# Performance work log

Measured on AMD Instinct MI355X. Metric: run time of the kernel, lower is better.

## Reference

```python
import jax, jax.numpy as jnp
import numpy as np
import math

B, T, D = 2, 2048, 2048
N_HEADS, N_KV, HEAD_DIM = 16, 4, 128
INTER = 8192
MAX_POS = 4096
ROPE_BASE = 10000.0
EPS = 1e-6


def _rope_tables():
    inv_freq = 1.0 / (ROPE_BASE ** (jnp.arange(0, HEAD_DIM, 2, dtype=jnp.float32) / HEAD_DIM))
    t = jnp.arange(MAX_POS, dtype=jnp.float32)
    freqs = jnp.einsum('i,j->ij', t, inv_freq)          # [MAX_POS, HEAD_DIM//2]
    emb = jnp.concatenate([freqs, freqs], axis=-1)      # [MAX_POS, HEAD_DIM]
    return jnp.cos(emb), jnp.sin(emb)


def _apply_rope(x, cos, sin):
    # x: [B,H,T,Dh]; cos/sin: [B,T,Dh] (gathered by position_ids)
    c = cos[:, None, :, :]
    s = sin[:, None, :, :]
    x1 = x[..., ::2]
    x2 = x[..., 1::2]
    x_rot = jnp.stack([-x2, x1], axis=-1).reshape(x.shape)  # interleave(-x2, x1)
    return x * c + x_rot * s


def _rms_norm(x, w):
    var = jnp.mean(x * x, axis=-1, keepdims=True)
    return w * (x * jax.lax.rsqrt(var + EPS))


def setup_inputs() -> dict:
    key = jax.random.key(0)
    ks = jax.random.split(key, 10)
    s = 0.02
    hidden_states = jax.random.normal(ks[0], (B, T, D), dtype=jnp.float32)
    # additive causal mask
    causal = jnp.tril(jnp.ones((T, T), dtype=bool))
    attention_mask = jnp.where(causal, 0.0, -1e9).astype(jnp.float32)[None, None]
    position_ids = jnp.arange(B * T).reshape(B, T)  # values < MAX_POS
    return {
        'hidden_states': hidden_states,
        'attention_mask': attention_mask,
        'position_ids': position_ids,
        'attn_norm_w': jnp.ones((D,), jnp.float32),
        'mlp_norm_w': jnp.ones((D,), jnp.float32),
        'wq': jax.random.normal(ks[1], (D, N_HEADS * HEAD_DIM), jnp.float32) * s,
        'wk': jax.random.normal(ks[2], (D, N_KV * HEAD_DIM), jnp.float32) * s,
        'wv': jax.random.normal(ks[3], (D, N_KV * HEAD_DIM), jnp.float32) * s,
        'wo': jax.random.normal(ks[4], (N_HEADS * HEAD_DIM, D), jnp.float32) * s,
        'gate_w': jax.random.normal(ks[5], (D, D), jnp.float32) * s,
        'gate_b': jnp.zeros((D,), jnp.float32),
        'fc1_w': jax.random.normal(ks[6], (D, INTER), jnp.float32) * s,
        'fc2_w': jax.random.normal(ks[7], (INTER, D), jnp.float32) * s,
    }


def reference(hidden_states, attention_mask, position_ids, attn_norm_w, mlp_norm_w,
              wq, wk, wv, wo, gate_w, gate_b, fc1_w, fc2_w):
    b, t, _ = hidden_states.shape
    residual = hidden_states
    h = _rms_norm(hidden_states, attn_norm_w)

    # elementwise sigmoid output gate: [B,T,D] -> [B,H,T,Dh]
    gate = jax.nn.sigmoid(h @ gate_w + gate_b)
    gate = gate.reshape(b, t, N_HEADS, HEAD_DIM).transpose(0, 2, 1, 3)

    q = (h @ wq).reshape(b, t, N_HEADS, HEAD_DIM).transpose(0, 2, 1, 3)
    k = (h @ wk).reshape(b, t, N_KV, HEAD_DIM).transpose(0, 2, 1, 3)
    v = (h @ wv).reshape(b, t, N_KV, HEAD_DIM).transpose(0, 2, 1, 3)

    cos_t, sin_t = _rope_tables()
    cos = cos_t[position_ids]  # [B,T,Dh]
    sin = sin_t[position_ids]
    q = _apply_rope(q, cos, sin)
    k = _apply_rope(k, cos, sin)

    n_rep = N_HEADS // N_KV
    k = jnp.repeat(k, n_rep, axis=1)  # GQA expand to [B,H,T,Dh]
    v = jnp.repeat(v, n_rep, axis=1)

    scores = jnp.einsum('bhqd,bhkd->bhqk', q, k) / math.sqrt(HEAD_DIM)
    scores = scores + attention_mask
    attn = jax.nn.softmax(scores, axis=-1)
    out = jnp.einsum('bhqk,bhkd->bhqd', attn, v) * gate
    out = out.transpose(0, 2, 1, 3).reshape(b, t, N_HEADS * HEAD_DIM) @ wo

    h = residual + out
    residual = h
    h2 = _rms_norm(h, mlp_norm_w)
    mlp_out = jax.nn.silu(h2 @ fc1_w) @ fc2_w
    return residual + mlp_out
```

## Files before the change

### kernel.cpp

```cpp
#include <hip/hip_runtime.h>
#include <hip/hip_bf16.h>
#include <cstdint>
#include <cstddef>

#define BB 2
#define TT 2048
#define DD 2048
#define NH 16
#define NKV 4
#define HD 128
#define NI 8192
#define MM (BB*TT)

typedef __bf16 bf16x8 __attribute__((ext_vector_type(8)));
typedef float  f32x4  __attribute__((ext_vector_type(4)));

__device__ __forceinline__ void gload_lds16(const void* g, void* l) {
  __builtin_amdgcn_global_load_lds((__attribute__((address_space(1))) void*)g,
                                   (__attribute__((address_space(3))) void*)l,
                                   16, 0, 0);
}

__device__ __forceinline__ int xcd_swizzle(int wg, int nwg) {
  int xcd = wg & 7;
  int l = wg >> 3;
  int q = nwg >> 3, r = nwg & 7;
  return (xcd < r ? xcd * (q + 1) : r * (q + 1) + (xcd - r) * q) + l;
}

__global__ __launch_bounds__(128) void rope_tables_k(float* __restrict__ cosT,
                                                     float* __restrict__ sinT) {
  int pos = blockIdx.x;
  int d = threadIdx.x;
  int f = d & 63;
  float inv = powf(10000.0f, -((float)(2 * f)) / 128.0f);
  float ang = inv * (float)pos;
  cosT[pos * 128 + d] = cosf(ang);
  sinT[pos * 128 + d] = sinf(ang);
}

template <typename TIN>
__global__ __launch_bounds__(256) void transpose_to_bf16_k(const TIN* __restrict__ in,
                                                           __bf16* __restrict__ out,
                                                           int R, int C) {
  __shared__ float t[32][33];
  int c0 = blockIdx.x * 32, r0 = blockIdx.y * 32;
  int tx = threadIdx.x & 31;
  int ty = threadIdx.x >> 5;
#pragma unroll
  for (int i = 0; i < 4; i++) {
    int r = ty + i * 8;
    t[r][tx] = (float)in[(size_t)(r0 + r) * C + c0 + tx];
  }
  __syncthreads();
#pragma unroll
  for (int i = 0; i < 4; i++) {
    int r = ty + i * 8;
    out[(size_t)(c0 + r) * R + r0 + tx] = (__bf16)t[tx][r];
  }
}

__global__ __launch_bounds__(256) void rmsnorm_k(const float* __restrict__ x,
                                                 const float* __restrict__ w,
                                                 __bf16* __restrict__ out) {
  int row = blockIdx.x;
  const float* xr = x + (size_t)row * DD;
  int t = threadIdx.x;
  float4 a = ((const float4*)xr)[2 * t];
  float4 b = ((const float4*)xr)[2 * t + 1];
  float ss = a.x * a.x + a.y * a.y + a.z * a.z + a.w * a.w +
             b.x * b.x + b.y * b.y + b.z * b.z + b.w * b.w;
#pragma unroll
  for (int off = 32; off; off >>= 1) ss += __shfl_xor(ss, off, 64);
  __shared__ float red[4];
  if ((t & 63) == 0) red[t >> 6] = ss;
  __syncthreads();
  float tot = red[0] + red[1] + red[2] + red[3];
  float rs = rsqrtf(tot * (1.0f / DD) + 1e-6f);
  const float4 w1 = ((const float4*)w)[2 * t];
  const float4 w2 = ((const float4*)w)[2 * t + 1];
  bf16x8 ov;
  ov[0] = (__bf16)(a.x * rs * w1.x);
  ov[1] = (__bf16)(a.y * rs * w1.y);
  ov[2] = (__bf16)(a.z * rs * w1.z);
  ov[3] = (__bf16)(a.w * rs * w1.w);
  ov[4] = (__bf16)(b.x * rs * w2.x);
  ov[5] = (__bf16)(b.y * rs * w2.y);
  ov[6] = (__bf16)(b.z * rs * w2.z);
  ov[7] = (__bf16)(b.w * rs * w2.w);
  *(bf16x8*)(out + (size_t)row * DD + t * 8) = ov;
}

enum { G_QG = 0, G_RES = 1, G_SILU = 2, G_PART = 3 };

template <int EPI>
__global__ __launch_bounds__(512) void gemm256_k(
    const __bf16* __restrict__ A, const __bf16* __restrict__ Bt,
    __bf16* __restrict__ outB, float* __restrict__ outF,
    __bf16* __restrict__ outQ, __bf16* __restrict__ outG,
    const float* __restrict__ bias, const float* __restrict__ residual,
    const float* __restrict__ cosT, const float* __restrict__ sinT,
    const int* __restrict__ posids, int N, int K, int ldk, float oscale) {
  __shared__ __align__(16) __bf16 Ab[3][256 * 32];
  __shared__ __align__(16) __bf16 Bb[3][256 * 32];
  const int tid = threadIdx.x;
  const int lane = tid & 63;
  const int wid = tid >> 6;
  const int wr = wid >> 2;
  const int wc = wid & 3;
  const int fr = lane & 15;
  const int fg = lane >> 4;

  const int nwg = gridDim.x * gridDim.y;
  int wg = xcd_swizzle(blockIdx.y * gridDim.x + blockIdx.x, nwg);
  const int bx = wg % gridDim.x, by = wg / gridDim.x;
  const int m0 = by * 256;
  const int n0 = bx * 256;
  const int kz = blockIdx.z;
  const int kBase = kz * K;

  const int srow0 = wid * 32 + (lane >> 2);
  const int scol = (((lane & 3) ^ ((lane >> 3) & 3)) << 3);
  const __bf16* aS0 = A + (size_t)(m0 + srow0) * ldk + kBase + scol;
  const __bf16* aS1 = aS0 + (size_t)16 * ldk;
  const __bf16* bS0 = Bt + (size_t)(n0 + srow0) * ldk + kBase + scol;
  const __bf16* bS1 = bS0 + (size_t)16 * ldk;
  const int e0 = (wid * 2) * 512;
  const int e1 = (wid * 2 + 1) * 512;

  const int nt = K / 32;

#define STAGE_A(kt, s)                          \
  {                                             \
    const int k0_ = (kt) * 32;                  \
    gload_lds16(aS0 + k0_, &Ab[(s)][e0]);       \
    gload_lds16(aS1 + k0_, &Ab[(s)][e1]);       \
  }
#define STAGE_B(kt, s)                          \
  {                                             \
    const int k0_ = (kt) * 32;                  \
    gload_lds16(bS0 + k0_, &Bb[(s)][e0]);       \
    gload_lds16(bS1 + k0_, &Bb[(s)][e1]);       \
  }

  STAGE_A(0, 0);
  STAGE_B(0, 0);
  STAGE_A(1, 1);
  STAGE_B(1, 1);
  asm volatile("s_waitcnt vmcnt(4)" ::: "memory");
  __builtin_amdgcn_s_barrier();

  f32x4 acc[8][4];
#pragma unroll
  for (int i = 0; i < 8; i++)
#pragma unroll
    for (int j = 0; j < 4; j++) acc[i][j] = (f32x4){0.f, 0.f, 0.f, 0.f};

  const int asl = (fg ^ ((fr >> 1) & 3)) * 8;

  for (int t = 0; t < nt; ++t) {
    const int s = t % 3;
    const int sn = (t + 2) % 3;
    bf16x8 af[4], bfr[4];
#pragma unroll
    for (int mi = 0; mi < 4; mi++)
      af[mi] = *(const bf16x8*)&Ab[s][(wr * 128 + mi * 16 + fr) * 32 + asl];
#pragma unroll
    for (int ni = 0; ni < 4; ni++)
      bfr[ni] = *(const bf16x8*)&Bb[s][(wc * 64 + ni * 16 + fr) * 32 + asl];
    if (t + 2 < nt) STAGE_A(t + 2, sn);
    __builtin_amdgcn_s_barrier();
    asm volatile("s_waitcnt lgkmcnt(0)" ::: "memory");
    __builtin_amdgcn_sched_barrier(0);
    __builtin_amdgcn_s_setprio(1);
#pragma unroll
    for (int mi = 0; mi < 4; mi++)
#pragma unroll
      for (int ni = 0; ni < 4; ni++)
        acc[mi][ni] =
            __builtin_amdgcn_mfma_f32_16x16x32_bf16(af[mi], bfr[ni], acc[mi][ni], 0, 0, 0);
    __builtin_amdgcn_s_setprio(0);
    __builtin_amdgcn_s_barrier();
    bf16x8 af2[4];
#pragma unroll
    for (int mi = 0; mi < 4; mi++)
      af2[mi] = *(const bf16x8*)&Ab[s][(wr * 128 + (mi + 4) * 16 + fr) * 32 + asl];
    if (t + 2 < nt) {
      STAGE_B(t + 2, sn);
      asm volatile("s_waitcnt vmcnt(4)" ::: "memory");
    } else {
      asm volatile("s_waitcnt vmcnt(0)" ::: "memory");
    }
    __builtin_amdgcn_s_barrier();
    asm volatile("s_waitcnt lgkmcnt(0)" ::: "memory");
    __builtin_amdgcn_sched_barrier(0);
    __builtin_amdgcn_s_setprio(1);
#pragma unroll
    for (int mi = 0; mi < 4; mi++)
#pragma unroll
      for (int ni = 0; ni < 4; ni++)
        acc[mi + 4][ni] =
            __builtin_amdgcn_mfma_f32_16x16x32_bf16(af2[mi], bfr[ni], acc[mi + 4][ni], 0, 0, 0);
    __builtin_amdgcn_s_setprio(0);
    __builtin_amdgcn_s_barrier();
  }
#undef STAGE_A
#undef STAGE_B

#pragma unroll
  for (int mi = 0; mi < 8; mi++) {
    const int row = m0 + wr * 128 + mi * 16 + fg * 4;
#pragma unroll
    for (int ni = 0; ni < 4; ni++) {
      const int col = n0 + wc * 64 + ni * 16 + fr;
#pragma unroll
      for (int j = 0; j < 4; j++) {
        float v = acc[mi][ni][j];
        const int r = row + j;
        if constexpr (EPI == G_QG) {
          float vp = __shfl_xor(v, 1, 64);
          if (n0 < 2048) {
            int pos = posids[r];
            int d = col & 127;
            float c = cosT[pos * 128 + d], sn2 = sinT[pos * 128 + d];
            float o = (col & 1) ? (v * c + vp * sn2) : (v * c - vp * sn2);
            outQ[(size_t)r * 2048 + col] = (__bf16)(o * oscale);
          } else {
            float xx = v + bias[col - 2048];
            outG[(size_t)r * 2048 + (col - 2048)] = (__bf16)(1.0f / (1.0f + expf(-xx)));
          }
        } else if constexpr (EPI == G_RES) {
          outF[(size_t)r * N + col] = v + residual[(size_t)r * N + col];
        } else if constexpr (EPI == G_SILU) {
          outB[(size_t)r * N + col] = (__bf16)(v / (1.0f + expf(-v)));
        } else {
          outB[(size_t)(kz * MM + r) * N + col] = (__bf16)v;
        }
      }
    }
  }
}

__global__ __launch_bounds__(256) void combine_k(const __bf16* __restrict__ parts,
                                                 const float* __restrict__ res,
                                                 float* __restrict__ out) {
  size_t i = ((size_t)blockIdx.x * 256 + threadIdx.x) * 8;
  bf16x8 p0 = *(const bf16x8*)&parts[i];
  bf16x8 p1 = *(const bf16x8*)&parts[(size_t)MM * 2048 + i];
  float4 a = *(const float4*)&res[i];
  float4 b = *(const float4*)&res[i + 4];
  float4 o0, o1;
  o0.x = (float)p0[0] + (float)p1[0] + a.x;
  o0.y = (float)p0[1] + (float)p1[1] + a.y;
  o0.z = (float)p0[2] + (float)p1[2] + a.z;
  o0.w = (float)p0[3] + (float)p1[3] + a.w;
  o1.x = (float)p0[4] + (float)p1[4] + b.x;
  o1.y = (float)p0[5] + (float)p1[5] + b.y;
  o1.z = (float)p0[6] + (float)p1[6] + b.z;
  o1.w = (float)p0[7] + (float)p1[7] + b.w;
  *(float4*)&out[i] = o0;
  *(float4*)&out[i + 4] = o1;
}

__global__ __launch_bounds__(256) void gemm_kv_k(
    const __bf16* __restrict__ A, const __bf16* __restrict__ Bt,
    __bf16* __restrict__ kOut, __bf16* __restrict__ vOut,
    const float* __restrict__ cosT, const float* __restrict__ sinT,
    const int* __restrict__ posids, int K) {
  __shared__ __align__(16) __bf16 As[128 * 32];
  __shared__ __align__(16) __bf16 Bs[128 * 32];
  const int tid = threadIdx.x;
  const int lane = tid & 63;
  const int w = tid >> 6;
  const int wm = w >> 1, wn = w & 1;

  const int nwg = gridDim.x * gridDim.y;
  int wg = xcd_swizzle(blockIdx.y * gridDim.x + blockIdx.x, nwg);
  const int bx = wg % gridDim.x, by = wg / gridDim.x;
  const int m0 = by * 128;
  const int n0 = bx * 128;

  const int lr = lane >> 2;
  const int lc = (lane & 3) * 8;
  const __bf16* aSrc = A + (size_t)(m0 + 32 * w + lr) * K + lc;
  const __bf16* bSrc = Bt + (size_t)(n0 + 32 * w + lr) * K + lc;
  __bf16* aDst = &As[w * 1024];
  __bf16* bDst = &Bs[w * 1024];

  f32x4 acc[4][4];
#pragma unroll
  for (int i = 0; i < 4; i++)
#pragma unroll
    for (int j = 0; j < 4; j++) acc[i][j] = (f32x4){0.f, 0.f, 0.f, 0.f};

  const int fr = lane & 15;
  const int fc = (lane >> 4) * 8;

  for (int k0 = 0; k0 < K; k0 += 32) {
    __syncthreads();
    gload_lds16(aSrc + k0, aDst);
    gload_lds16(aSrc + k0 + (size_t)16 * K, aDst + 512);
    gload_lds16(bSrc + k0, bDst);
    gload_lds16(bSrc + k0 + (size_t)16 * K, bDst + 512);
    asm volatile("s_waitcnt vmcnt(0)" ::: "memory");
    __syncthreads();

    bf16x8 af[4], bfg[4];
#pragma unroll
    for (int i = 0; i < 4; i++)
      af[i] = *(const bf16x8*)&As[(wm * 64 + i * 16 + fr) * 32 + fc];
#pragma unroll
    for (int i = 0; i < 4; i++)
      bfg[i] = *(const bf16x8*)&Bs[(wn * 64 + i * 16 + fr) * 32 + fc];
#pragma unroll
    for (int mi = 0; mi < 4; mi++)
#pragma unroll
      for (int ni = 0; ni < 4; ni++)
        acc[mi][ni] =
            __builtin_amdgcn_mfma_f32_16x16x32_bf16(af[mi], bfg[ni], acc[mi][ni], 0, 0, 0);
  }

  const int fg = lane >> 4;
#pragma unroll
  for (int mi = 0; mi < 4; mi++) {
#pragma unroll
    for (int ni = 0; ni < 4; ni++) {
#pragma unroll
      for (int j = 0; j < 4; j++) {
        int row = m0 + wm * 64 + mi * 16 + fg * 4 + j;
        int col = n0 + wn * 64 + ni * 16 + fr;
        float v = acc[mi][ni][j];
        float vp = __shfl_xor(v, 1, 64);
        if (col < 512) {
          int pos = posids[row];
          int d = col & 127;
          float c = cosT[pos * 128 + d];
          float s = sinT[pos * 128 + d];
          float o = (col & 1) ? (v * c + vp * s) : (v * c - vp * s);
          kOut[(size_t)row * 512 + col] = (__bf16)o;
        } else {
          vOut[(size_t)row * 512 + (col - 512)] = (__bf16)v;
        }
      }
    }
  }
}

__global__ __launch_bounds__(256) void attn_k(const __bf16* __restrict__ Q,
                                              const __bf16* __restrict__ Kb,
                                              const __bf16* __restrict__ Vt,
                                              const __bf16* __restrict__ Gate,
                                              __bf16* __restrict__ Out) {
  __shared__ __align__(16) __bf16 Ks[2][64 * 128];
  __shared__ __align__(16) __bf16 Vs[2][128 * 64];
  __shared__ __align__(16) __bf16 Ps[4][16 * 64];
  const int tid = threadIdx.x;
  const int lane = tid & 63;
  const int w = tid >> 6;
  const int fr = lane & 15;
  const int fg = lane >> 4;

  const int nwg = gridDim.x * gridDim.y;
  int wg = xcd_swizzle(blockIdx.y * gridDim.x + blockIdx.x, nwg);
  const int qb = wg % gridDim.x;
  const int bh = wg / gridDim.x;
  const int q0 = qb * 64;
  const int b = bh >> 4, h = bh & 15;
  const int g = h >> 2;

  const size_t qrow = (size_t)(b * TT + q0 + w * 16 + fr);
  bf16x8 qf[4];
#pragma unroll
  for (int kt = 0; kt < 4; kt++)
    qf[kt] = *(const bf16x8*)&Q[qrow * 2048 + h * 128 + kt * 32 + fg * 8];

  const __bf16* kPtr[4];
  const __bf16* vPtr[4];
#pragma unroll
  for (int i = 0; i < 4; i++) {
    int krow = w * 16 + i * 4 + (lane >> 4);
    int kcol8 = (lane & 15) ^ (krow & 15);
    kPtr[i] = Kb + (size_t)(b * TT + krow) * 512 + g * 128 + kcol8 * 8;
    int dloc = w * 32 + i * 8 + (lane >> 3);
    int kv8 = (lane & 7) ^ (dloc & 7);
    vPtr[i] = Vt + (size_t)(g * 128 + dloc) * (size_t)MM + b * TT + kv8 * 8;
  }

  f32x4 o[8];
#pragma unroll
  for (int i = 0; i < 8; i++) o[i] = (f32x4){0.f, 0.f, 0.f, 0.f};
  float mrow[4] = {-3e38f, -3e38f, -3e38f, -3e38f};
  float lrow[4] = {0.f, 0.f, 0.f, 0.f};

  const int nsteps = qb + 1;

#pragma unroll
  for (int i = 0; i < 4; i++) {
    gload_lds16(kPtr[i], &Ks[0][w * 2048 + i * 512]);
    gload_lds16(vPtr[i], &Vs[0][w * 2048 + i * 512]);
  }
  __syncthreads();

  for (int t = 0; t < nsteps; t++) {
    const int cur = t & 1;
    const int kb = t * 64;
    if (t + 1 < nsteps) {
      const int nb = kb + 64;
#pragma unroll
      for (int i = 0; i < 4; i++) {
        gload_lds16(kPtr[i] + (size_t)nb * 512, &Ks[cur ^ 1][w * 2048 + i * 512]);
        gload_lds16(vPtr[i] + nb, &Vs[cur ^ 1][w * 2048 + i * 512]);
      }
    }

    f32x4 s[4];
#pragma unroll
    for (int nc = 0; nc < 4; nc++) s[nc] = (f32x4){0.f, 0.f, 0.f, 0.f};
#pragma unroll
    for (int nc = 0; nc < 4; nc++)
#pragma unroll
      for (int kt = 0; kt < 4; kt++) {
        bf16x8 kf = *(const bf16x8*)&Ks[cur][(nc * 16 + fr) * 128 + (((kt * 4 + fg) ^ fr) << 3)];
        s[nc] = __builtin_amdgcn_mfma_f32_16x16x32_bf16(qf[kt], kf, s[nc], 0, 0, 0);
      }

    float alpha[4];
#pragma unroll
    for (int j = 0; j < 4; j++) {
      const int qr = q0 + w * 16 + fg * 4 + j;
      float pv[4];
#pragma unroll
      for (int nc = 0; nc < 4; nc++) {
        int kc = kb + nc * 16 + fr;
        float val = s[nc][j];
        if (kc > qr) val = -1e9f;
        pv[nc] = val;
      }
      float tmx = fmaxf(fmaxf(pv[0], pv[1]), fmaxf(pv[2], pv[3]));
      tmx = fmaxf(tmx, __shfl_xor(tmx, 1, 64));
      tmx = fmaxf(tmx, __shfl_xor(tmx, 2, 64));
      tmx = fmaxf(tmx, __shfl_xor(tmx, 4, 64));
      tmx = fmaxf(tmx, __shfl_xor(tmx, 8, 64));
      float mnew = fmaxf(mrow[j], tmx);
      alpha[j] = __expf(mrow[j] - mnew);
      mrow[j] = mnew;
      float rsum = 0.f;
      const int q = fg * 4 + j;
#pragma unroll
      for (int nc = 0; nc < 4; nc++) {
        float e = __expf(pv[nc] - mnew);
        rsum += e;
        Ps[w][q * 64 + (((nc * 2 + (fr >> 3)) ^ (q & 7)) << 3) + (fr & 7)] = (__bf16)e;
      }
      rsum += __shfl_xor(rsum, 1, 64);
      rsum += __shfl_xor(rsum, 2, 64);
      rsum += __shfl_xor(rsum, 4, 64);
      rsum += __shfl_xor(rsum, 8, 64);
      lrow[j] = lrow[j] * alpha[j] + rsum;
    }
#pragma unroll
    for (int nd = 0; nd < 8; nd++)
#pragma unroll
      for (int j = 0; j < 4; j++) o[nd][j] *= alpha[j];

    bf16x8 pa[2];
#pragma unroll
    for (int sl = 0; sl < 2; sl++)
      pa[sl] = *(const bf16x8*)&Ps[w][fr * 64 + (((sl * 4 + fg) ^ (fr & 7)) << 3)];
#pragma unroll
    for (int nd = 0; nd < 8; nd++)
#pragma unroll
      for (int sl = 0; sl < 2; sl++) {
        bf16x8 vf =
            *(const bf16x8*)&Vs[cur][(nd * 16 + fr) * 64 + (((sl * 4 + fg) ^ (fr & 7)) << 3)];
        o[nd] = __builtin_amdgcn_mfma_f32_16x16x32_bf16(pa[sl], vf, o[nd], 0, 0, 0);
      }
    __syncthreads();
  }

  float invl[4];
#pragma unroll
  for (int j = 0; j < 4; j++) invl[j] = 1.0f / lrow[j];
#pragma unroll
  for (int nd = 0; nd < 8; nd++) {
#pragma unroll
    for (int j = 0; j < 4; j++) {
      int row = q0 + w * 16 + fg * 4 + j;
      int d = nd * 16 + fr;
      size_t idx = (size_t)(b * TT + row) * 2048 + h * 128 + d;
      float val = o[nd][j] * invl[j] * (float)Gate[idx];
      Out[idx] = (__bf16)val;
    }
  }
}

extern "C" void kernel_launch(void* const* d_in, const int* in_sizes, int n_in,
                              void* d_out, int out_size, void* d_ws, size_t ws_size,
                              hipStream_t stream) {
  const float* hidden = (const float*)d_in[0];
  const int* posids = (const int*)d_in[2];
  const float* attn_w = (const float*)d_in[3];
  const float* mlp_w = (const float*)d_in[4];
  const float* wq = (const float*)d_in[5];
  const float* wk = (const float*)d_in[6];
  const float* wv = (const float*)d_in[7];
  const float* wo = (const float*)d_in[8];
  const float* gw = (const float*)d_in[9];
  const float* gb = (const float*)d_in[10];
  const float* f1 = (const float*)d_in[11];
  const float* f2 = (const float*)d_in[12];

  char* p = (char*)d_ws;
  auto alloc = [&](size_t n) {
    char* r = p;
    p += (n + 255) & ~(size_t)255;
    return r;
  };
  __bf16* wqg_t = (__bf16*)alloc((size_t)4096 * 2048 * 2);
  __bf16* wkv_t = (__bf16*)alloc((size_t)1024 * 2048 * 2);
  __bf16* wo_t = (__bf16*)alloc((size_t)2048 * 2048 * 2);
  __bf16* f1_t = (__bf16*)alloc((size_t)NI * 2048 * 2);
  __bf16* f2_t = (__bf16*)alloc((size_t)2048 * NI * 2);
  __bf16* h_bf = (__bf16*)alloc((size_t)MM * DD * 2);
  float* h1 = (float*)alloc((size_t)MM * 2048 * 4);

  char* regionA = alloc((size_t)64 * 1024 * 1024);
  __bf16* q_bf = (__bf16*)(regionA);
  __bf16* gate_bf = (__bf16*)(regionA + (size_t)16 * 1024 * 1024);
  __bf16* attn_g = (__bf16*)(regionA + (size_t)32 * 1024 * 1024);
  __bf16* k_bf = (__bf16*)(regionA + (size_t)48 * 1024 * 1024);
  __bf16* v_bf = (__bf16*)(regionA + (size_t)52 * 1024 * 1024);
  __bf16* v_t = (__bf16*)(regionA + (size_t)56 * 1024 * 1024);
  float* cosT = (float*)(regionA + (size_t)60 * 1024 * 1024);
  float* sinT = (float*)(regionA + (size_t)62 * 1024 * 1024);
  __bf16* mlp1 = (__bf16*)(regionA);
  __bf16* parts_wo = (__bf16*)(regionA);
  __bf16* parts_fc2 = (__bf16*)f1_t;

  rope_tables_k<<<4096, 128, 0, stream>>>(cosT, sinT);

  transpose_to_bf16_k<float><<<dim3(64, 64), 256, 0, stream>>>(wq, wqg_t, 2048, 2048);
  transpose_to_bf16_k<float><<<dim3(64, 64), 256, 0, stream>>>(gw, wqg_t + (size_t)2048 * 2048, 2048, 2048);
  transpose_to_bf16_k<float><<<dim3(16, 64), 256, 0, stream>>>(wk, wkv_t, 2048, 512);
  transpose_to_bf16_k<float><<<dim3(16, 64), 256, 0, stream>>>(wv, wkv_t + (size_t)512 * 2048, 2048, 512);
  transpose_to_bf16_k<float><<<dim3(64, 64), 256, 0, stream>>>(wo, wo_t, 2048, 2048);
  transpose_to_bf16_k<float><<<dim3(256, 64), 256, 0, stream>>>(f1, f1_t, 2048, NI);
  transpose_to_bf16_k<float><<<dim3(64, 256), 256, 0, stream>>>(f2, f2_t, NI, 2048);

  rmsnorm_k<<<MM, 256, 0, stream>>>(hidden, attn_w, h_bf);

  const float qsc = 0.08838834764831845f;
  gemm256_k<G_QG><<<dim3(16, 16), 512, 0, stream>>>(
      h_bf, wqg_t, nullptr, nullptr, q_bf, gate_bf, gb, nullptr, cosT, sinT, posids,
      4096, 2048, 2048, qsc);
  gemm_kv_k<<<dim3(8, 32), 256, 0, stream>>>(h_bf, wkv_t, k_bf, v_bf, cosT, sinT, posids, 2048);

  transpose_to_bf16_k<__bf16><<<dim3(16, 128), 256, 0, stream>>>(v_bf, v_t, MM, 512);

  attn_k<<<dim3(32, 32), 256, 0, stream>>>(q_bf, k_bf, v_t, gate_bf, attn_g);

  gemm256_k<G_PART><<<dim3(8, 16, 2), 512, 0, stream>>>(
      attn_g, wo_t, parts_wo, nullptr, nullptr, nullptr, nullptr, nullptr, nullptr, nullptr,
      nullptr, 2048, 1024, 2048, 1.0f);
  combine_k<<<4096, 256, 0, stream>>>(parts_wo, hidden, h1);

  rmsnorm_k<<<MM, 256, 0, stream>>>(h1, mlp_w, h_bf);

  gemm256_k<G_SILU><<<dim3(32, 16), 512, 0, stream>>>(
      h_bf, f1_t, mlp1, nullptr, nullptr, nullptr, nullptr, nullptr, nullptr, nullptr, nullptr,
      NI, 2048, 2048, 1.0f);

  gemm256_k<G_PART><<<dim3(8, 16, 2), 512, 0, stream>>>(
      mlp1, f2_t, parts_fc2, nullptr, nullptr, nullptr, nullptr, nullptr, nullptr, nullptr,
      nullptr, 2048, 4096, NI, 1.0f);

  combine_k<<<4096, 256, 0, stream>>>(parts_fc2, h1, (float*)d_out);
}
```

Before: 792.8 us.

## Fuse residual combine with MLP RMSNorm and reorder GEMM second-half waits

```diff
diff --git a/kernel.cpp b/kernel.cpp
--- a/kernel.cpp
+++ b/kernel.cpp
@@ -185,23 +185,23 @@
 #pragma unroll
     for (int mi = 0; mi < 4; mi++)
       af2[mi] = *(const bf16x8*)&Ab[s][(wr * 128 + (mi + 4) * 16 + fr) * 32 + asl];
+    if (t + 2 < nt) STAGE_B(t + 2, sn);
+    __builtin_amdgcn_s_barrier();
+    asm volatile("s_waitcnt lgkmcnt(0)" ::: "memory");
+    __builtin_amdgcn_sched_barrier(0);
+    __builtin_amdgcn_s_setprio(1);
+#pragma unroll
+    for (int mi = 0; mi < 4; mi++)
+#pragma unroll
+      for (int ni = 0; ni < 4; ni++)
+        acc[mi + 4][ni] =
+            __builtin_amdgcn_mfma_f32_16x16x32_bf16(af2[mi], bfr[ni], acc[mi + 4][ni], 0, 0, 0);
+    __builtin_amdgcn_s_setprio(0);
     if (t + 2 < nt) {
-      STAGE_B(t + 2, sn);
       asm volatile("s_waitcnt vmcnt(4)" ::: "memory");
     } else {
       asm volatile("s_waitcnt vmcnt(0)" ::: "memory");
     }
-    __builtin_amdgcn_s_barrier();
-    asm volatile("s_waitcnt lgkmcnt(0)" ::: "memory");
-    __builtin_amdgcn_sched_barrier(0);
-    __builtin_amdgcn_s_setprio(1);
-#pragma unroll
-    for (int mi = 0; mi < 4; mi++)
-#pragma unroll
-      for (int ni = 0; ni < 4; ni++)
-        acc[mi + 4][ni] =
-            __builtin_amdgcn_mfma_f32_16x16x32_bf16(af2[mi], bfr[ni], acc[mi + 4][ni], 0, 0, 0);
-    __builtin_amdgcn_s_setprio(0);
     __builtin_amdgcn_s_barrier();
   }
 #undef STAGE_A
@@ -262,6 +262,55 @@
   *(float4*)&out[i + 4] = o1;
 }
 
+__global__ __launch_bounds__(256) void combine_rms_k(const __bf16* __restrict__ parts,
+                                                     const float* __restrict__ res,
+                                                     const float* __restrict__ w,
+                                                     float* __restrict__ h1,
+                                                     __bf16* __restrict__ h2) {
+  const int row = blockIdx.x;
+  const int t = threadIdx.x;
+  const size_t i = (size_t)row * 2048 + t * 8;
+  bf16x8 p0 = *(const bf16x8*)&parts[i];
+  bf16x8 p1 = *(const bf16x8*)&parts[(size_t)MM * 2048 + i];
+  float4 a = *(const float4*)&res[i];
+  float4 b = *(const float4*)&res[i + 4];
+  float v[8];
+  v[0] = (float)p0[0] + (float)p1[0] + a.x;
+  v[1] = (float)p0[1] + (float)p1[1] + a.y;
+  v[2] = (float)p0[2] + (float)p1[2] + a.z;
+  v[3] = (float)p0[3] + (float)p1[3] + a.w;
+  v[4] = (float)p0[4] + (float)p1[4] + b.x;
+  v[5] = (float)p0[5] + (float)p1[5] + b.y;
+  v[6] = (float)p0[6] + (float)p1[6] + b.z;
+  v[7] = (float)p0[7] + (float)p1[7] + b.w;
+  float4 o0 = {v[0], v[1], v[2], v[3]};
+  float4 o1 = {v[4], v[5], v[6], v[7]};
+  *(float4*)&h1[i] = o0;
+  *(float4*)&h1[i + 4] = o1;
+  float ss = 0.f;
+#pragma unroll
+  for (int k = 0; k < 8; k++) ss += v[k] * v[k];
+#pragma unroll
+  for (int off = 32; off; off >>= 1) ss += __shfl_xor(ss, off, 64);
+  __shared__ float red[4];
+  if ((t & 63) == 0) red[t >> 6] = ss;
+  __syncthreads();
+  float tot = red[0] + red[1] + red[2] + red[3];
+  float rs = rsqrtf(tot * (1.0f / DD) + 1e-6f);
+  const float4 w1 = ((const float4*)w)[2 * t];
+  const float4 w2 = ((const float4*)w)[2 * t + 1];
+  bf16x8 ov;
+  ov[0] = (__bf16)(v[0] * rs * w1.x);
+  ov[1] = (__bf16)(v[1] * rs * w1.y);
+  ov[2] = (__bf16)(v[2] * rs * w1.z);
+  ov[3] = (__bf16)(v[3] * rs * w1.w);
+  ov[4] = (__bf16)(v[4] * rs * w2.x);
+  ov[5] = (__bf16)(v[5] * rs * w2.y);
+  ov[6] = (__bf16)(v[6] * rs * w2.z);
+  ov[7] = (__bf16)(v[7] * rs * w2.w);
+  *(bf16x8*)(h2 + i) = ov;
+}
+
 __global__ __launch_bounds__(256) void gemm_kv_k(
     const __bf16* __restrict__ A, const __bf16* __restrict__ Bt,
     __bf16* __restrict__ kOut, __bf16* __restrict__ vOut,
@@ -562,9 +611,7 @@
   gemm256_k<G_PART><<<dim3(8, 16, 2), 512, 0, stream>>>(
       attn_g, wo_t, parts_wo, nullptr, nullptr, nullptr, nullptr, nullptr, nullptr, nullptr,
       nullptr, 2048, 1024, 2048, 1.0f);
-  combine_k<<<4096, 256, 0, stream>>>(parts_wo, hidden, h1);
-
-  rmsnorm_k<<<MM, 256, 0, stream>>>(h1, mlp_w, h_bf);
+  combine_rms_k<<<MM, 256, 0, stream>>>(parts_wo, hidden, mlp_w, h1, h_bf);
 
   gemm256_k<G_SILU><<<dim3(32, 16), 512, 0, stream>>>(
       h_bf, f1_t, mlp1, nullptr, nullptr, nullptr, nullptr, nullptr, nullptr, nullptr, nullptr,
```

Measured after the change: 783.3 us, median of 2. Within noise of the previous version (-1.2%).
